# Optimization experiments

Measured on AMD Instinct MI355X. Metric: run time of the kernel, lower is better.

## Reference

```python
import jax, jax.numpy as jnp
import numpy as np

LN_EPS = 1e-5


def layer_norm(x, gamma, beta):
    mu = jnp.mean(x, axis=-1, keepdims=True)
    var = jnp.var(x, axis=-1, keepdims=True)
    return (x - mu) * jax.lax.rsqrt(var + LN_EPS) * gamma + beta


def setup_inputs() -> dict:
    key = jax.random.key(0)
    ks = jax.random.split(key, 8)
    d = 768
    B, H, W = 8, 32, 32
    s = 1.0 / np.sqrt(d)
    inp = {
        "x": jax.random.normal(ks[0], (B, d, H, W), dtype=jnp.float32),
        "Wq": jax.random.normal(ks[1], (d, d), dtype=jnp.float32) * s,
        "bq": jnp.zeros((d,), jnp.float32),
        "Wk": jax.random.normal(ks[2], (d, d), dtype=jnp.float32) * s,
        "bk": jnp.zeros((d,), jnp.float32),
        "Wv": jax.random.normal(ks[3], (d, d), dtype=jnp.float32) * s,
        "bv": jnp.zeros((d,), jnp.float32),
        "Wo": jax.random.normal(ks[4], (d, d), dtype=jnp.float32) * s,
        "bo": jnp.zeros((d,), jnp.float32),
        "Wg": jax.random.normal(ks[5], (d, d), dtype=jnp.float32) * s,
        "bg": jnp.zeros((d,), jnp.float32),
        "gamma": jnp.ones((d,), jnp.float32),
        "beta": jnp.zeros((d,), jnp.float32),
    }
    return inp


def reference(x, Wq, bq, Wk, bk, Wv, bv, Wo, bo, Wg, bg, gamma, beta):
    n_heads = 12
    B, C, H, W = x.shape
    T = H * W
    d_head = C // n_heads
    # (B, C, H, W) -> (B, T, C)
    xt = x.reshape(B, C, T).transpose(0, 2, 1)
    xn = layer_norm(xt, gamma, beta)
    # torch Linear: x @ W.T + b
    q = xn @ Wq.T + bq
    k = xn @ Wk.T + bk
    v = xn @ Wv.T + bv

    def split_heads(t):
        return t.reshape(B, T, n_heads, d_head).transpose(0, 2, 1, 3)  # (B, nH, T, dh)

    q, k, v = split_heads(q), split_heads(k), split_heads(v)
    scale = 1.0 / np.sqrt(d_head).astype(np.float32)
    scores = jnp.einsum("bhtd,bhsd->bhts", q, k) * scale  # (B, nH, T, T)
    probs = jax.nn.softmax(scores, axis=-1)
    y = jnp.einsum("bhts,bhsd->bhtd", probs, v)  # (B, nH, T, dh)
    # headwise + elementwise gate over full d_model
    gate = jax.nn.sigmoid(xn @ Wg.T + bg)  # (B, T, C)
    gate = gate.reshape(B, T, n_heads, d_head).transpose(0, 2, 1, 3)
    y = y * gate
    y = y.transpose(0, 2, 1, 3).reshape(B, T, C)
    out = y @ Wo.T + bo  # (B, T, C)
    return out.transpose(0, 2, 1).reshape(B, C, H, W)
```

## Files before the change

kernel.cpp:

```cpp
#include <hip/hip_runtime.h>
#include <math.h>

#define B_   8
#define C_   768
#define T_   1024
#define BT_  (B_*T_)
#define WSZ  (C_*C_)

using f16x8 = __attribute__((ext_vector_type(8))) _Float16;
using f32x4 = __attribute__((ext_vector_type(4))) float;
typedef unsigned short u16;

__device__ inline u16 f16b(float x) {
    _Float16 h = (_Float16)x;
    return __builtin_bit_cast(u16, h);
}
__device__ inline float f16f(u16 b) {
    return (float)__builtin_bit_cast(_Float16, b);
}

__global__ __launch_bounds__(256) void wconv_all(
    const float* __restrict__ W0, const float* __restrict__ W1,
    const float* __restrict__ W2, const float* __restrict__ W3,
    const float* __restrict__ W4, u16* __restrict__ wbuf) {
    int mat = blockIdx.y;
    const float* W = (mat == 0) ? W0 : (mat == 1) ? W1 : (mat == 2) ? W2
                   : (mat == 3) ? W3 : W4;
    u16* o = wbuf + (size_t)mat * WSZ;
    int i = (blockIdx.x * 256 + threadIdx.x) * 4;
    float4 w = *(const float4*)(W + i);
    ushort4 h;
    h.x = f16b(w.x);
    h.y = f16b(w.y);
    h.z = f16b(w.z);
    h.w = f16b(w.w);
    *(ushort4*)(o + i) = h;
}

__global__ __launch_bounds__(256) void ln_kernel(const float* __restrict__ x,
                                                 const float* __restrict__ gamma,
                                                 const float* __restrict__ beta,
                                                 u16* __restrict__ xh) {
    int row = blockIdx.x;
    int b = row >> 10;
    int t = row & 1023;
    int tid = threadIdx.x;
    const float* xb = x + (size_t)b * C_ * T_ + t;
    float v0 = xb[(size_t)(tid      ) * T_];
    float v1 = xb[(size_t)(tid + 256) * T_];
    float v2 = xb[(size_t)(tid + 512) * T_];
    float s  = v0 + v1 + v2;
    float sq = v0 * v0 + v1 * v1 + v2 * v2;
    #pragma unroll
    for (int m = 1; m < 64; m <<= 1) {
        s  += __shfl_xor(s,  m);
        sq += __shfl_xor(sq, m);
    }
    __shared__ float ss[4], ssq[4];
    int wid = tid >> 6;
    if ((tid & 63) == 0) { ss[wid] = s; ssq[wid] = sq; }
    __syncthreads();
    s  = ss[0] + ss[1] + ss[2] + ss[3];
    sq = ssq[0] + ssq[1] + ssq[2] + ssq[3];
    float mu   = s * (1.0f / 768.0f);
    float var  = sq * (1.0f / 768.0f) - mu * mu;
    float rstd = 1.0f / sqrtf(var + 1e-5f);
    size_t o = (size_t)row * C_;
    xh[o + tid      ] = f16b((v0 - mu) * rstd * gamma[tid      ] + beta[tid      ]);
    xh[o + tid + 256] = f16b((v1 - mu) * rstd * gamma[tid + 256] + beta[tid + 256]);
    xh[o + tid + 512] = f16b((v2 - mu) * rstd * gamma[tid + 512] + beta[tid + 512]);
}

__global__ __launch_bounds__(256, 3) void qkvg_mfma(
    const u16* __restrict__ xh, const u16* __restrict__ wmats,
    const float* __restrict__ bq, const float* __restrict__ bk,
    const float* __restrict__ bv, const float* __restrict__ bg,
    u16* __restrict__ qh, u16* __restrict__ kh,
    u16* __restrict__ vth, u16* __restrict__ g) {
    int bx = blockIdx.x;
    int by = blockIdx.y;
    int mat = by / 6;
    int n0  = (by % 6) * 128;
    int m0  = bx * 128;
    const u16* Wh = wmats + (size_t)mat * WSZ;
    const float* bias = (mat == 0) ? bq : (mat == 1) ? bk : (mat == 2) ? bv : bg;

    __shared__ __attribute__((aligned(16))) u16 Ah[2 * 4096], Bh[2 * 4096];

    int tid  = threadIdx.x;
    int lane = tid & 63, wid = tid >> 6;
    int wm = (wid & 1) * 64, wn = (wid >> 1) * 64;
    int fr = lane & 15, rq = (lane >> 4) * 4;

    f32x4 acc[4][4];
    #pragma unroll
    for (int i = 0; i < 4; ++i)
        #pragma unroll
        for (int j = 0; j < 4; ++j)
            acc[i][j] = (f32x4){0.f, 0.f, 0.f, 0.f};

    int j = tid >> 5, u = tid & 31;
    size_t offA = (size_t)(m0 + j * 16 + (u & 15)) * 768 + (u >> 4) * 8;
    size_t offB = (size_t)(n0 + j * 16 + (u & 15)) * 768 + (u >> 4) * 8;
    int lo0 = j * 512 + u * 8;
    int ba = (wm >> 4), bb2 = (wn >> 4);

    uint4 a0, a1, c0, c1;
    #define LOADT(T) do { int kk0 = (T) * 32; \
        a0 = *(const uint4*)(xh + offA + kk0); \
        a1 = *(const uint4*)(xh + offA + kk0 + 16); \
        c0 = *(const uint4*)(Wh + offB + kk0); \
        c1 = *(const uint4*)(Wh + offB + kk0 + 16); \
    } while (0)
    #define STORET(BUF) do { int lb = (BUF) * 4096 + lo0; \
        *(uint4*)(Ah + lb) = a0;  *(uint4*)(Ah + lb + 256) = a1; \
        *(uint4*)(Bh + lb) = c0;  *(uint4*)(Bh + lb + 256) = c1; \
    } while (0)

    LOADT(0);
    STORET(0);
    LOADT(1);
    __syncthreads();
    int cur = 0;
    for (int t = 0; t < 24; ++t) {
        int nxt = cur ^ 1;
        STORET(nxt);
        LOADT((t + 2 < 24) ? t + 2 : 0);
        int cb = cur * 4096;
        f16x8 fah[4], fbh[4];
        #pragma unroll
        for (int i = 0; i < 4; ++i) {
            fah[i] = *(const f16x8*)(Ah + cb + (ba + i) * 512 + lane * 8);
            fbh[i] = *(const f16x8*)(Bh + cb + (bb2 + i) * 512 + lane * 8);
        }
        if (mat == 2) {
            #pragma unroll
            for (int mi = 0; mi < 4; ++mi)
                #pragma unroll
                for (int ni = 0; ni < 4; ++ni)
                    acc[mi][ni] = __builtin_amdgcn_mfma_f32_16x16x32_f16(fbh[ni], fah[mi], acc[mi][ni], 0, 0, 0);
        } else {
            #pragma unroll
            for (int mi = 0; mi < 4; ++mi)
                #pragma unroll
                for (int ni = 0; ni < 4; ++ni)
                    acc[mi][ni] = __builtin_amdgcn_mfma_f32_16x16x32_f16(fah[mi], fbh[ni], acc[mi][ni], 0, 0, 0);
        }
        __syncthreads();
        cur = nxt;
    }
    #undef LOADT
    #undef STORET
    if (mat == 2) {
        int bb = m0 >> 10;
        #pragma unroll
        for (int mi = 0; mi < 4; ++mi) {
            int tok = m0 + wm + mi * 16 + fr;
            int tl  = tok & 1023;
            #pragma unroll
            for (int ni = 0; ni < 4; ++ni) {
                #pragma unroll
                for (int rg = 0; rg < 4; ++rg) {
                    int ch = n0 + wn + ni * 16 + rq + rg;
                    float val = acc[mi][ni][rg] + bias[ch];
                    size_t addr = ((size_t)((bb * 12 + (ch >> 6)) * 64 + (ch & 63))) * 1024 + tl;
                    vth[addr] = f16b(val);
                }
            }
        }
    } else {
        u16* oh = (mat == 0) ? qh : (mat == 1) ? kh : g;
        float scale = (mat == 0) ? 0.125f : 1.0f;
        #pragma unroll
        for (int ni = 0; ni < 4; ++ni) {
            int col = n0 + wn + ni * 16 + fr;
            float bb = bias[col];
            #pragma unroll
            for (int mi = 0; mi < 4; ++mi) {
                int row = m0 + wm + mi * 16 + rq;
                #pragma unroll
                for (int rg = 0; rg < 4; ++rg) {
                    float val = (acc[mi][ni][rg] + bb) * scale;
                    oh[(size_t)(row + rg) * 768 + col] = f16b(val);
                }
            }
        }
    }
}

__global__ __launch_bounds__(256, 3) void attn_mfma(
    const u16* __restrict__ qhg, const u16* __restrict__ khg,
    const u16* __restrict__ vthg, const u16* __restrict__ gbf,
    u16* __restrict__ yh) {
    int qt = blockIdx.x;
    int h  = blockIdx.y;
    int b  = blockIdx.z;
    __shared__ u16 Kh[2 * 4096], Vh[2 * 4096];
    __shared__ u16 Ps[64 * 72];
    int tid = threadIdx.x;
    int lane = tid & 63, w = tid >> 6;
    int fr = lane & 15, quad = lane >> 4, fq = quad * 8;

    size_t qbase = ((size_t)(b * 1024 + qt * 64)) * 768 + h * 64;
    size_t kbase = ((size_t)(b * 1024)) * 768 + h * 64;
    size_t vbase = ((size_t)((b * 12 + h) * 64)) * 1024;

    f16x8 aq[2];
    #pragma unroll
    for (int kk = 0; kk < 2; ++kk)
        aq[kk] = *(const f16x8*)(qhg + qbase + (size_t)(w * 16 + fr) * 768 + kk * 32 + fq);

    float m_s = -1e30f, l_s = 0.0f;
    f32x4 Oacc[4];
    #pragma unroll
    for (int i = 0; i < 4; ++i) Oacc[i] = (f32x4){0.f, 0.f, 0.f, 0.f};

    int j = tid >> 5, u = tid & 31;
    int kk_ = j >> 2, nd_ = j & 3;
    size_t offK = kbase + (size_t)(nd_ * 16 + (u & 15)) * 768 + kk_ * 32 + (u >> 4) * 8;
    size_t offV = vbase + (size_t)(nd_ * 16 + (u & 15)) * 1024 + kk_ * 32 + (u >> 4) * 8;
    int lo0 = j * 512 + u * 8;

    uint4 rk0, rk1, rv0, rv1;
    #define LOADKV(ST) do { \
        size_t ok = offK + (size_t)(ST) * 49152; \
        size_t ov = offV + (size_t)(ST) * 64; \
        rk0 = *(const uint4*)(khg + ok);  rk1 = *(const uint4*)(khg + ok + 16); \
        rv0 = *(const uint4*)(vthg + ov); rv1 = *(const uint4*)(vthg + ov + 16); \
    } while (0)
    #define STOREKV(BUF) do { \
        int lb = (BUF) * 4096 + lo0; \
        *(uint4*)(Kh + lb) = rk0;  *(uint4*)(Kh + lb + 256) = rk1; \
        *(uint4*)(Vh + lb) = rv0;  *(uint4*)(Vh + lb + 256) = rv1; \
    } while (0)

    LOADKV(0);
    STOREKV(0);
    LOADKV(1);
    __syncthreads();
    int cur = 0;
    for (int st = 0; st < 16; ++st) {
        int nxt = cur ^ 1;
        STOREKV(nxt);
        int s2 = (st + 2 < 16) ? (st + 2) : 0;
        LOADKV(s2);
        f32x4 sacc[4];
        #pragma unroll
        for (int nt = 0; nt < 4; ++nt) sacc[nt] = (f32x4){0.f, 0.f, 0.f, 0.f};
        #pragma unroll
        for (int nt = 0; nt < 4; ++nt)
            #pragma unroll
            for (int kk = 0; kk < 2; ++kk) {
                f16x8 kb = *(const f16x8*)(Kh + cur * 4096 + (kk * 4 + nt) * 512 + lane * 8);
                sacc[nt] = __builtin_amdgcn_mfma_f32_16x16x32_f16(kb, aq[kk], sacc[nt], 0, 0, 0);
            }
        float mx = -1e30f;
        #pragma unroll
        for (int nt = 0; nt < 4; ++nt)
            #pragma unroll
            for (int rg = 0; rg < 4; ++rg) mx = fmaxf(mx, sacc[nt][rg]);
        mx = fmaxf(mx, __shfl_xor(mx, 16));
        mx = fmaxf(mx, __shfl_xor(mx, 32));
        float mn = fmaxf(m_s, mx);
        float al = __expf(m_s - mn);
        m_s = mn;
        float rs = 0.0f;
        #pragma unroll
        for (int nt = 0; nt < 4; ++nt)
            #pragma unroll
            for (int rg = 0; rg < 4; ++rg) {
                float p = __expf(sacc[nt][rg] - mn);
                sacc[nt][rg] = p;
                rs += p;
            }
        rs += __shfl_xor(rs, 16);
        rs += __shfl_xor(rs, 32);
        l_s = l_s * al + rs;
        int prow = (w * 16 + fr) * 72;
        #pragma unroll
        for (int nt = 0; nt < 4; ++nt) {
            ushort4 hp;
            hp.x = f16b(sacc[nt][0]);
            hp.y = f16b(sacc[nt][1]);
            hp.z = f16b(sacc[nt][2]);
            hp.w = f16b(sacc[nt][3]);
            *(ushort4*)&Ps[prow + nt * 16 + quad * 4] = hp;
        }
        float alr[4];
        #pragma unroll
        for (int rg = 0; rg < 4; ++rg) alr[rg] = __shfl(al, quad * 4 + rg, 16);
        #pragma unroll
        for (int dn = 0; dn < 4; ++dn)
            #pragma unroll
            for (int rg = 0; rg < 4; ++rg) Oacc[dn][rg] *= alr[rg];
        #pragma unroll
        for (int kk = 0; kk < 2; ++kk) {
            f16x8 pa = *(const f16x8*)&Ps[(w * 16 + fr) * 72 + fq + kk * 32];
            #pragma unroll
            for (int dn = 0; dn < 4; ++dn) {
                f16x8 vb = *(const f16x8*)(Vh + cur * 4096 + (kk * 4 + dn) * 512 + lane * 8);
                Oacc[dn] = __builtin_amdgcn_mfma_f32_16x16x32_f16(pa, vb, Oacc[dn], 0, 0, 0);
            }
        }
        __syncthreads();
        cur = nxt;
    }
    #undef LOADKV
    #undef STOREKV
    float inv[4];
    #pragma unroll
    for (int rg = 0; rg < 4; ++rg) inv[rg] = 1.0f / __shfl(l_s, quad * 4 + rg, 16);
    #pragma unroll
    for (int dn = 0; dn < 4; ++dn) {
        int ch = h * 64 + dn * 16 + fr;
        #pragma unroll
        for (int rg = 0; rg < 4; ++rg) {
            int tok = b * 1024 + qt * 64 + w * 16 + quad * 4 + rg;
            float gv = f16f(gbf[(size_t)tok * 768 + ch]);
            float sg = 1.0f / (1.0f + __expf(-gv));
            float val = Oacc[dn][rg] * inv[rg] * sg;
            yh[(size_t)tok * 768 + ch] = f16b(val);
        }
    }
}

__global__ __launch_bounds__(256, 3) void out_mfma(
    const u16* __restrict__ yh, const u16* __restrict__ woh,
    const float* __restrict__ bo, float* __restrict__ out) {
    int bx = blockIdx.x;
    int by = blockIdx.y;
    int m0 = bx * 128;
    int n0 = by * 128;

    __shared__ __attribute__((aligned(16))) u16 Ah[2 * 4096], Bh[2 * 4096];

    int tid  = threadIdx.x;
    int lane = tid & 63, wid = tid >> 6;
    int wm = (wid & 1) * 64, wn = (wid >> 1) * 64;
    int fr = lane & 15, rq = (lane >> 4) * 4;

    f32x4 acc[4][4];
    #pragma unroll
    for (int i = 0; i < 4; ++i)
        #pragma unroll
        for (int j = 0; j < 4; ++j)
            acc[i][j] = (f32x4){0.f, 0.f, 0.f, 0.f};

    int j = tid >> 5, u = tid & 31;
    size_t offA = (size_t)(m0 + j * 16 + (u & 15)) * 768 + (u >> 4) * 8;
    size_t offB = (size_t)(n0 + j * 16 + (u & 15)) * 768 + (u >> 4) * 8;
    int lo0 = j * 512 + u * 8;
    int ba = (wm >> 4), bb2 = (wn >> 4);

    uint4 a0, a1, c0, c1;
    #define LOADT(T) do { int kk0 = (T) * 32; \
        a0 = *(const uint4*)(woh + offA + kk0); \
        a1 = *(const uint4*)(woh + offA + kk0 + 16); \
        c0 = *(const uint4*)(yh + offB + kk0); \
        c1 = *(const uint4*)(yh + offB + kk0 + 16); \
    } while (0)
    #define STORET(BUF) do { int lb = (BUF) * 4096 + lo0; \
        *(uint4*)(Ah + lb) = a0;  *(uint4*)(Ah + lb + 256) = a1; \
        *(uint4*)(Bh + lb) = c0;  *(uint4*)(Bh + lb + 256) = c1; \
    } while (0)

    LOADT(0);
    STORET(0);
    LOADT(1);
    __syncthreads();
    int cur = 0;
    for (int t = 0; t < 24; ++t) {
        int nxt = cur ^ 1;
        STORET(nxt);
        LOADT((t + 2 < 24) ? t + 2 : 0);
        int cb = cur * 4096;
        f16x8 fah[4], fbh[4];
        #pragma unroll
        for (int i = 0; i < 4; ++i) {
            fah[i] = *(const f16x8*)(Ah + cb + (ba + i) * 512 + lane * 8);
            fbh[i] = *(const f16x8*)(Bh + cb + (bb2 + i) * 512 + lane * 8);
        }
        #pragma unroll
        for (int mi = 0; mi < 4; ++mi)
            #pragma unroll
            for (int ni = 0; ni < 4; ++ni)
                acc[mi][ni] = __builtin_amdgcn_mfma_f32_16x16x32_f16(fah[mi], fbh[ni], acc[mi][ni], 0, 0, 0);
        __syncthreads();
        cur = nxt;
    }
    #undef LOADT
    #undef STORET
    int bb = n0 >> 10;
    #pragma unroll
    for (int ni = 0; ni < 4; ++ni) {
        int colg = n0 + wn + ni * 16 + fr;
        int tl = colg & 1023;
        #pragma unroll
        for (int mi = 0; mi < 4; ++mi) {
            int row = m0 + wm + mi * 16 + rq;
            #pragma unroll
            for (int rg = 0; rg < 4; ++rg) {
                float val = acc[mi][ni][rg] + bo[row + rg];
                out[((size_t)bb * 768 + row + rg) * 1024 + tl] = val;
            }
        }
    }
}

extern "C" void kernel_launch(void* const* d_in, const int* in_sizes, int n_in,
                              void* d_out, int out_size, void* d_ws, size_t ws_size,
                              hipStream_t stream) {
    const float* x     = (const float*)d_in[0];
    const float* Wq    = (const float*)d_in[1];
    const float* bq    = (const float*)d_in[2];
    const float* Wk    = (const float*)d_in[3];
    const float* bk    = (const float*)d_in[4];
    const float* Wv    = (const float*)d_in[5];
    const float* bv    = (const float*)d_in[6];
    const float* Wo    = (const float*)d_in[7];
    const float* bo    = (const float*)d_in[8];
    const float* Wg    = (const float*)d_in[9];
    const float* bg    = (const float*)d_in[10];
    const float* gamma = (const float*)d_in[11];
    const float* beta  = (const float*)d_in[12];
    float* out = (float*)d_out;

    const size_t S = (size_t)BT_ * C_;
    u16* xn   = (u16*)d_ws;
    u16* qh   = xn + S;
    u16* kh   = qh + S;
    u16* vth  = kh + S;
    u16* g_bf = vth + S;
    u16* wbuf = g_bf + S;
    u16* y_h  = xn;

    wconv_all<<<dim3(WSZ / 1024, 5), 256, 0, stream>>>(Wq, Wk, Wv, Wg, Wo, wbuf);
    ln_kernel<<<BT_, 256, 0, stream>>>(x, gamma, beta, xn);
    qkvg_mfma<<<dim3(64, 24), 256, 0, stream>>>(xn, wbuf, bq, bk, bv, bg,
                                                qh, kh, vth, g_bf);
    attn_mfma<<<dim3(16, 12, 8), 256, 0, stream>>>(qh, kh, vth, g_bf, y_h);
    out_mfma<<<dim3(6, 64), 256, 0, stream>>>(y_h, wbuf + (size_t)4 * WSZ, bo, out);
}
```

Baseline: 321.9 us.

## Load GEMM A operands directly to registers and tile LayerNorm over tokens

The LayerNorm kernel now handles 16 tokens per block, so reads along the token axis are coalesced across 16 threads. It stages the normalized rows in shared memory so the row-major f16 output is written with vector stores. Both projection GEMMs drop the shared-memory A tile: each wave loads its A fragments straight from global memory into double-buffered registers, and only B goes through LDS. This cuts LDS traffic and store instructions, at the cost of more registers, which is why launch bounds drop from 3 to 2 blocks per SM.

```diff
diff --git a/kernel.cpp b/kernel.cpp
--- a/kernel.cpp
+++ b/kernel.cpp
@@ -41,37 +41,53 @@
                                                  const float* __restrict__ gamma,
                                                  const float* __restrict__ beta,
                                                  u16* __restrict__ xh) {
-    int row = blockIdx.x;
-    int b = row >> 10;
-    int t = row & 1023;
+    int b = blockIdx.y;
+    int t0 = blockIdx.x * 16;
     int tid = threadIdx.x;
-    const float* xb = x + (size_t)b * C_ * T_ + t;
-    float v0 = xb[(size_t)(tid      ) * T_];
-    float v1 = xb[(size_t)(tid + 256) * T_];
-    float v2 = xb[(size_t)(tid + 512) * T_];
-    float s  = v0 + v1 + v2;
-    float sq = v0 * v0 + v1 * v1 + v2 * v2;
-    #pragma unroll
-    for (int m = 1; m < 64; m <<= 1) {
-        s  += __shfl_xor(s,  m);
-        sq += __shfl_xor(sq, m);
-    }
-    __shared__ float ss[4], ssq[4];
-    int wid = tid >> 6;
-    if ((tid & 63) == 0) { ss[wid] = s; ssq[wid] = sq; }
-    __syncthreads();
-    s  = ss[0] + ss[1] + ss[2] + ss[3];
-    sq = ssq[0] + ssq[1] + ssq[2] + ssq[3];
-    float mu   = s * (1.0f / 768.0f);
-    float var  = sq * (1.0f / 768.0f) - mu * mu;
-    float rstd = 1.0f / sqrtf(var + 1e-5f);
-    size_t o = (size_t)row * C_;
-    xh[o + tid      ] = f16b((v0 - mu) * rstd * gamma[tid      ] + beta[tid      ]);
-    xh[o + tid + 256] = f16b((v1 - mu) * rstd * gamma[tid + 256] + beta[tid + 256]);
-    xh[o + tid + 512] = f16b((v2 - mu) * rstd * gamma[tid + 512] + beta[tid + 512]);
-}
-
-__global__ __launch_bounds__(256, 3) void qkvg_mfma(
+    int tx = tid & 15;
+    int cg = tid >> 4;
+    const float* xb = x + (size_t)b * C_ * T_ + t0 + tx;
+
+    float v[48];
+    float s = 0.f, sq = 0.f;
+    #pragma unroll
+    for (int i = 0; i < 48; ++i) {
+        float val = xb[(size_t)(i * 16 + cg) * T_];
+        v[i] = val; s += val; sq += val * val;
+    }
+    __shared__ float rs_[16][16], rq_[16][16];
+    rs_[cg][tx] = s;
+    rq_[cg][tx] = sq;
+    __syncthreads();
+    __shared__ float mu_[16], rstd_[16];
+    if (tid < 16) {
+        float S = 0.f, Q = 0.f;
+        #pragma unroll
+        for (int k = 0; k < 16; ++k) { S += rs_[k][tid]; Q += rq_[k][tid]; }
+        float mu = S * (1.0f / 768.0f);
+        float var = Q * (1.0f / 768.0f) - mu * mu;
+        mu_[tid] = mu;
+        rstd_[tid] = 1.0f / sqrtf(var + 1e-5f);
+    }
+    __syncthreads();
+    float mu = mu_[tx], rstd = rstd_[tx];
+    __shared__ u16 Lt[16][776];
+    #pragma unroll
+    for (int i = 0; i < 48; ++i) {
+        int c = i * 16 + cg;
+        Lt[tx][c] = f16b((v[i] - mu) * rstd * gamma[c] + beta[c]);
+    }
+    __syncthreads();
+    size_t obase = ((size_t)b * 1024 + t0) * C_;
+    #pragma unroll
+    for (int st = 0; st < 12; ++st) {
+        int idx = st * 256 + tid;
+        int t = idx / 192, c4 = idx % 192;
+        *(ushort4*)(xh + obase + (size_t)t * C_ + c4 * 4) = *(ushort4*)&Lt[t][c4 * 4];
+    }
+}
+
+__global__ __launch_bounds__(256, 2) void qkvg_mfma(
     const u16* __restrict__ xh, const u16* __restrict__ wmats,
     const float* __restrict__ bq, const float* __restrict__ bk,
     const float* __restrict__ bv, const float* __restrict__ bg,
@@ -85,7 +101,7 @@
     const u16* Wh = wmats + (size_t)mat * WSZ;
     const float* bias = (mat == 0) ? bq : (mat == 1) ? bk : (mat == 2) ? bv : bg;
 
-    __shared__ __attribute__((aligned(16))) u16 Ah[2 * 4096], Bh[2 * 4096];
+    __shared__ __attribute__((aligned(16))) u16 Bh[2 * 4096];
 
     int tid  = threadIdx.x;
     int lane = tid & 63, wid = tid >> 6;
@@ -100,57 +116,68 @@
             acc[i][j] = (f32x4){0.f, 0.f, 0.f, 0.f};
 
     int j = tid >> 5, u = tid & 31;
-    size_t offA = (size_t)(m0 + j * 16 + (u & 15)) * 768 + (u >> 4) * 8;
     size_t offB = (size_t)(n0 + j * 16 + (u & 15)) * 768 + (u >> 4) * 8;
     int lo0 = j * 512 + u * 8;
-    int ba = (wm >> 4), bb2 = (wn >> 4);
-
-    uint4 a0, a1, c0, c1;
-    #define LOADT(T) do { int kk0 = (T) * 32; \
-        a0 = *(const uint4*)(xh + offA + kk0); \
-        a1 = *(const uint4*)(xh + offA + kk0 + 16); \
+    int bb2 = (wn >> 4);
+
+    const u16* Arow = xh + (size_t)(m0 + wm + fr) * 768 + (lane >> 4) * 8;
+
+    uint4 c0, c1;
+    f16x8 aA[4], aB[4];
+    #define LOADB(T) do { int kk0 = (T) * 32; \
         c0 = *(const uint4*)(Wh + offB + kk0); \
         c1 = *(const uint4*)(Wh + offB + kk0 + 16); \
     } while (0)
-    #define STORET(BUF) do { int lb = (BUF) * 4096 + lo0; \
-        *(uint4*)(Ah + lb) = a0;  *(uint4*)(Ah + lb + 256) = a1; \
+    #define STOREB(BUF) do { int lb = (BUF) * 4096 + lo0; \
         *(uint4*)(Bh + lb) = c0;  *(uint4*)(Bh + lb + 256) = c1; \
     } while (0)
-
-    LOADT(0);
-    STORET(0);
-    LOADT(1);
+    #define LOADA(dst, T) do { int kk0 = (T) * 32; \
+        dst[0] = *(const f16x8*)(Arow + kk0); \
+        dst[1] = *(const f16x8*)(Arow + 12288 + kk0); \
+        dst[2] = *(const f16x8*)(Arow + 24576 + kk0); \
+        dst[3] = *(const f16x8*)(Arow + 36864 + kk0); \
+    } while (0)
+    #define BODY(AREG, T) do { \
+        STOREB(cur ^ 1); \
+        LOADB(((T) + 2 < 24) ? (T) + 2 : 0); \
+        int cb = cur * 4096; \
+        if (mat == 2) { \
+            _Pragma("unroll") \
+            for (int ni = 0; ni < 4; ++ni) { \
+                f16x8 fb = *(const f16x8*)(Bh + cb + (bb2 + ni) * 512 + lane * 8); \
+                _Pragma("unroll") \
+                for (int mi = 0; mi < 4; ++mi) \
+                    acc[mi][ni] = __builtin_amdgcn_mfma_f32_16x16x32_f16(fb, AREG[mi], acc[mi][ni], 0, 0, 0); \
+            } \
+        } else { \
+            _Pragma("unroll") \
+            for (int ni = 0; ni < 4; ++ni) { \
+                f16x8 fb = *(const f16x8*)(Bh + cb + (bb2 + ni) * 512 + lane * 8); \
+                _Pragma("unroll") \
+                for (int mi = 0; mi < 4; ++mi) \
+                    acc[mi][ni] = __builtin_amdgcn_mfma_f32_16x16x32_f16(AREG[mi], fb, acc[mi][ni], 0, 0, 0); \
+            } \
+        } \
+        LOADA(AREG, ((T) + 2 < 24) ? (T) + 2 : 0); \
+        __syncthreads(); \
+        cur ^= 1; \
+    } while (0)
+
+    LOADB(0);
+    STOREB(0);
+    LOADB(1);
+    LOADA(aA, 0);
+    LOADA(aB, 1);
     __syncthreads();
     int cur = 0;
-    for (int t = 0; t < 24; ++t) {
-        int nxt = cur ^ 1;
-        STORET(nxt);
-        LOADT((t + 2 < 24) ? t + 2 : 0);
-        int cb = cur * 4096;
-        f16x8 fah[4], fbh[4];
-        #pragma unroll
-        for (int i = 0; i < 4; ++i) {
-            fah[i] = *(const f16x8*)(Ah + cb + (ba + i) * 512 + lane * 8);
-            fbh[i] = *(const f16x8*)(Bh + cb + (bb2 + i) * 512 + lane * 8);
-        }
-        if (mat == 2) {
-            #pragma unroll
-            for (int mi = 0; mi < 4; ++mi)
-                #pragma unroll
-                for (int ni = 0; ni < 4; ++ni)
-                    acc[mi][ni] = __builtin_amdgcn_mfma_f32_16x16x32_f16(fbh[ni], fah[mi], acc[mi][ni], 0, 0, 0);
-        } else {
-            #pragma unroll
-            for (int mi = 0; mi < 4; ++mi)
-                #pragma unroll
-                for (int ni = 0; ni < 4; ++ni)
-                    acc[mi][ni] = __builtin_amdgcn_mfma_f32_16x16x32_f16(fah[mi], fbh[ni], acc[mi][ni], 0, 0, 0);
-        }
-        __syncthreads();
-        cur = nxt;
-    }
-    #undef LOADT
-    #undef STORET
+    for (int t = 0; t < 24; t += 2) {
+        BODY(aA, t);
+        BODY(aB, t + 1);
+    }
+    #undef LOADB
+    #undef STOREB
+    #undef LOADA
+    #undef BODY
     if (mat == 2) {
         int bb = m0 >> 10;
         #pragma unroll
@@ -324,7 +351,7 @@
     }
 }
 
-__global__ __launch_bounds__(256, 3) void out_mfma(
+__global__ __launch_bounds__(256, 2) void out_mfma(
     const u16* __restrict__ yh, const u16* __restrict__ woh,
     const float* __restrict__ bo, float* __restrict__ out) {
     int bx = blockIdx.x;
@@ -332,7 +359,7 @@
     int m0 = bx * 128;
     int n0 = by * 128;
 
-    __shared__ __attribute__((aligned(16))) u16 Ah[2 * 4096], Bh[2 * 4096];
+    __shared__ __attribute__((aligned(16))) u16 Bh[2 * 4096];
 
     int tid  = threadIdx.x;
     int lane = tid & 63, wid = tid >> 6;
@@ -347,49 +374,58 @@
             acc[i][j] = (f32x4){0.f, 0.f, 0.f, 0.f};
 
     int j = tid >> 5, u = tid & 31;
-    size_t offA = (size_t)(m0 + j * 16 + (u & 15)) * 768 + (u >> 4) * 8;
     size_t offB = (size_t)(n0 + j * 16 + (u & 15)) * 768 + (u >> 4) * 8;
     int lo0 = j * 512 + u * 8;
-    int ba = (wm >> 4), bb2 = (wn >> 4);
-
-    uint4 a0, a1, c0, c1;
-    #define LOADT(T) do { int kk0 = (T) * 32; \
-        a0 = *(const uint4*)(woh + offA + kk0); \
-        a1 = *(const uint4*)(woh + offA + kk0 + 16); \
+    int bb2 = (wn >> 4);
+
+    const u16* Arow = woh + (size_t)(m0 + wm + fr) * 768 + (lane >> 4) * 8;
+
+    uint4 c0, c1;
+    f16x8 aA[4], aB[4];
+    #define LOADB(T) do { int kk0 = (T) * 32; \
         c0 = *(const uint4*)(yh + offB + kk0); \
         c1 = *(const uint4*)(yh + offB + kk0 + 16); \
     } while (0)
-    #define STORET(BUF) do { int lb = (BUF) * 4096 + lo0; \
-        *(uint4*)(Ah + lb) = a0;  *(uint4*)(Ah + lb + 256) = a1; \
+    #define STOREB(BUF) do { int lb = (BUF) * 4096 + lo0; \
         *(uint4*)(Bh + lb) = c0;  *(uint4*)(Bh + lb + 256) = c1; \
     } while (0)
-
-    LOADT(0);
-    STORET(0);
-    LOADT(1);
+    #define LOADA(dst, T) do { int kk0 = (T) * 32; \
+        dst[0] = *(const f16x8*)(Arow + kk0); \
+        dst[1] = *(const f16x8*)(Arow + 12288 + kk0); \
+        dst[2] = *(const f16x8*)(Arow + 24576 + kk0); \
+        dst[3] = *(const f16x8*)(Arow + 36864 + kk0); \
+    } while (0)
+    #define BODY(AREG, T) do { \
+        STOREB(cur ^ 1); \
+        LOADB(((T) + 2 < 24) ? (T) + 2 : 0); \
+        int cb = cur * 4096; \
+        _Pragma("unroll") \
+        for (int ni = 0; ni < 4; ++ni) { \
+            f16x8 fb = *(const f16x8*)(Bh + cb + (bb2 + ni) * 512 + lane * 8); \
+            _Pragma("unroll") \
+            for (int mi = 0; mi < 4; ++mi) \
+                acc[mi][ni] = __builtin_amdgcn_mfma_f32_16x16x32_f16(AREG[mi], fb, acc[mi][ni], 0, 0, 0); \
+        } \
+        LOADA(AREG, ((T) + 2 < 24) ? (T) + 2 : 0); \
+        __syncthreads(); \
+        cur ^= 1; \
+    } while (0)
+
+    LOADB(0);
+    STOREB(0);
+    LOADB(1);
+    LOADA(aA, 0);
+    LOADA(aB, 1);
     __syncthreads();
     int cur = 0;
-    for (int t = 0; t < 24; ++t) {
-        int nxt = cur ^ 1;
-        STORET(nxt);
-        LOADT((t + 2 < 24) ? t + 2 : 0);
-        int cb = cur * 4096;
-        f16x8 fah[4], fbh[4];
-        #pragma unroll
-        for (int i = 0; i < 4; ++i) {
-            fah[i] = *(const f16x8*)(Ah + cb + (ba + i) * 512 + lane * 8);
-            fbh[i] = *(const f16x8*)(Bh + cb + (bb2 + i) * 512 + lane * 8);
-        }
-        #pragma unroll
-        for (int mi = 0; mi < 4; ++mi)
-            #pragma unroll
-            for (int ni = 0; ni < 4; ++ni)
-                acc[mi][ni] = __builtin_amdgcn_mfma_f32_16x16x32_f16(fah[mi], fbh[ni], acc[mi][ni], 0, 0, 0);
-        __syncthreads();
-        cur = nxt;
-    }
-    #undef LOADT
-    #undef STORET
+    for (int t = 0; t < 24; t += 2) {
+        BODY(aA, t);
+        BODY(aB, t + 1);
+    }
+    #undef LOADB
+    #undef STOREB
+    #undef LOADA
+    #undef BODY
     int bb = n0 >> 10;
     #pragma unroll
     for (int ni = 0; ni < 4; ++ni) {
@@ -435,7 +471,7 @@
     u16* y_h  = xn;
 
     wconv_all<<<dim3(WSZ / 1024, 5), 256, 0, stream>>>(Wq, Wk, Wv, Wg, Wo, wbuf);
-    ln_kernel<<<BT_, 256, 0, stream>>>(x, gamma, beta, xn);
+    ln_kernel<<<dim3(64, 8), 256, 0, stream>>>(x, gamma, beta, xn);
     qkvg_mfma<<<dim3(64, 24), 256, 0, stream>>>(xn, wbuf, bq, bk, bv, bg,
                                                 qh, kh, vth, g_bf);
     attn_mfma<<<dim3(16, 12, 8), 256, 0, stream>>>(qh, kh, vth, g_bf, y_h);
```

After: 318.4 us. No clear change (-1.1%).
